# Performance work log

Hardware: AMD Instinct MI355X
Metric: run time of the kernel (lower is better)

Reference implementation:

```python
import jax, jax.numpy as jnp
import numpy as np


def _gcn_conv(x, edge_index, W, b):
    # PyG GCNConv: linear transform, add self-loops, symmetric deg^{-1/2} norm,
    # scatter-add aggregation from source (row) into target (col), then bias.
    N = x.shape[0]
    h = x @ W  # [N, out]
    loops = jnp.arange(N, dtype=edge_index.dtype)
    row = jnp.concatenate([edge_index[0], loops])  # sources j
    col = jnp.concatenate([edge_index[1], loops])  # targets i
    deg = jax.ops.segment_sum(jnp.ones_like(col, dtype=h.dtype), col, num_segments=N)
    dinv = jnp.where(deg > 0, jax.lax.rsqrt(deg), 0.0)
    norm = dinv[row] * dinv[col]  # [E+N]
    msgs = norm[:, None] * h[row]  # gather + scale
    out = jax.ops.segment_sum(msgs, col, num_segments=N)  # scatter-add
    return out + b


def setup_inputs() -> dict:
    key = jax.random.key(0)
    k1, k2, k3, k4 = jax.random.split(key, 4)
    N, E, F, H = 100000, 3200000, 128, 64
    x = jax.random.normal(k1, (N, F), dtype=jnp.float32)
    edge_index = jax.random.randint(k2, (2, E), 0, N, dtype=jnp.int64)
    W1 = jax.random.normal(k3, (F, H), dtype=jnp.float32) * (1.0 / np.sqrt(F))
    b1 = jnp.zeros((H,), dtype=jnp.float32)
    W2 = jax.random.normal(k4, (H, 1), dtype=jnp.float32) * (1.0 / np.sqrt(H))
    b2 = jnp.zeros((1,), dtype=jnp.float32)
    return {"x": x, "edge_index": edge_index, "W1": W1, "b1": b1, "W2": W2, "b2": b2}


def reference(x, edge_index, W1, b1, W2, b2):
    # eval mode: dropout is identity
    h = _gcn_conv(x, edge_index, W1, b1)
    h = jax.nn.relu(h)
    h = _gcn_conv(h, edge_index, W2, b2)  # [N, 1]
    return jnp.mean(h, axis=0)  # [1]
```

## Files before the change

kernel.cpp:

```cpp
#include <hip/hip_runtime.h>
#include <hip/hip_bf16.h>
#include <stdint.h>


#define F_IN 128
#define H_DIM 64
#define BKT_SH 7
#define BKT_SZ 128
#define MAXBKT 1024
#define PWG 128
#define PTHR 256
#define FINBLK 2048

typedef int   i4 __attribute__((ext_vector_type(4)));
typedef float f4 __attribute__((ext_vector_type(4)));

__device__ __forceinline__ float2 bfp(unsigned int u) {
    return make_float2(__uint_as_float(u << 16), __uint_as_float(u & 0xffff0000u));
}

__global__ __launch_bounds__(PTHR) void k_hist1(const int* __restrict__ col,
                                                int* __restrict__ histG,
                                                int E, int nbkt, int chunk) {
    __shared__ int h[MAXBKT];
    for (int i = threadIdx.x; i < nbkt; i += PTHR) h[i] = 0;
    __syncthreads();
    int s = blockIdx.x * chunk, e = min(E, s + chunk);
    if (s < e) {
        int s4 = s >> 2, e4 = e >> 2;
        const i4* c4 = (const i4*)col;
        int t = s4 + threadIdx.x;
        for (; t + 3 * PTHR < e4; t += 4 * PTHR) {
            i4 a = __builtin_nontemporal_load(c4 + t);
            i4 b = __builtin_nontemporal_load(c4 + t + PTHR);
            i4 c = __builtin_nontemporal_load(c4 + t + 2 * PTHR);
            i4 d = __builtin_nontemporal_load(c4 + t + 3 * PTHR);
            atomicAdd(&h[a.x >> BKT_SH], 1); atomicAdd(&h[a.y >> BKT_SH], 1);
            atomicAdd(&h[a.z >> BKT_SH], 1); atomicAdd(&h[a.w >> BKT_SH], 1);
            atomicAdd(&h[b.x >> BKT_SH], 1); atomicAdd(&h[b.y >> BKT_SH], 1);
            atomicAdd(&h[b.z >> BKT_SH], 1); atomicAdd(&h[b.w >> BKT_SH], 1);
            atomicAdd(&h[c.x >> BKT_SH], 1); atomicAdd(&h[c.y >> BKT_SH], 1);
            atomicAdd(&h[c.z >> BKT_SH], 1); atomicAdd(&h[c.w >> BKT_SH], 1);
            atomicAdd(&h[d.x >> BKT_SH], 1); atomicAdd(&h[d.y >> BKT_SH], 1);
            atomicAdd(&h[d.z >> BKT_SH], 1); atomicAdd(&h[d.w >> BKT_SH], 1);
        }
        for (; t < e4; t += PTHR) {
            i4 a = __builtin_nontemporal_load(c4 + t);
            atomicAdd(&h[a.x >> BKT_SH], 1); atomicAdd(&h[a.y >> BKT_SH], 1);
            atomicAdd(&h[a.z >> BKT_SH], 1); atomicAdd(&h[a.w >> BKT_SH], 1);
        }
        for (int i = (e4 << 2) + threadIdx.x; i < e; i += PTHR)
            atomicAdd(&h[col[i] >> BKT_SH], 1);
    }
    __syncthreads();
    for (int i = threadIdx.x; i < nbkt; i += PTHR)
        histG[(size_t)i * PWG + blockIdx.x] = h[i];
}

__global__ __launch_bounds__(PWG) void k_hscan_a(int* __restrict__ histG,
                                                 int* __restrict__ total, int nbkt) {
    __shared__ int s[PWG];
    int b = blockIdx.x, t = threadIdx.x;
    int v = histG[(size_t)b * PWG + t];
    s[t] = v;
    __syncthreads();
    for (int d = 1; d < PWG; d <<= 1) {
        int a = (t >= d) ? s[t - d] : 0;
        __syncthreads();
        s[t] += a;
        __syncthreads();
    }
    histG[(size_t)b * PWG + t] = s[t] - v;
    if (t == PWG - 1) total[b] = s[t];
}

__global__ __launch_bounds__(1024) void k_hscan_b(const int* __restrict__ total,
                                                  int* __restrict__ bstart, int nbkt) {
    __shared__ int s[1024];
    int t = threadIdx.x;
    int v = (t < nbkt) ? total[t] : 0;
    s[t] = v;
    __syncthreads();
    for (int d = 1; d < 1024; d <<= 1) {
        int a = (t >= d) ? s[t - d] : 0;
        __syncthreads();
        s[t] += a;
        __syncthreads();
    }
    if (t < nbkt) bstart[t] = s[t] - v;
    if (t == nbkt - 1) bstart[nbkt] = s[t];
}

__global__ __launch_bounds__(PTHR) void k_part(const int* __restrict__ row,
                                               const int* __restrict__ col,
                                               const int* __restrict__ histG,
                                               const int* __restrict__ bstart,
                                               unsigned int* __restrict__ part,
                                               int E, int nbkt, int chunk) {
    __shared__ int cur[MAXBKT];
    for (int i = threadIdx.x; i < nbkt; i += PTHR)
        cur[i] = bstart[i] + histG[(size_t)i * PWG + blockIdx.x];
    __syncthreads();
    int s = blockIdx.x * chunk, e = min(E, s + chunk);
    if (s >= e) return;
    int s4 = s >> 2, e4 = e >> 2;
    const i4* c4 = (const i4*)col;
    const i4* r4 = (const i4*)row;
    int t = s4 + threadIdx.x;
    for (; t + PTHR < e4; t += 2 * PTHR) {
        i4 ca = __builtin_nontemporal_load(c4 + t);
        i4 ra = __builtin_nontemporal_load(r4 + t);
        i4 cb = __builtin_nontemporal_load(c4 + t + PTHR);
        i4 rb = __builtin_nontemporal_load(r4 + t + PTHR);
        int p;
        p = atomicAdd(&cur[ca.x >> BKT_SH], 1);
        part[p] = ((unsigned int)ra.x << BKT_SH) | (unsigned int)(ca.x & (BKT_SZ - 1));
        p = atomicAdd(&cur[ca.y >> BKT_SH], 1);
        part[p] = ((unsigned int)ra.y << BKT_SH) | (unsigned int)(ca.y & (BKT_SZ - 1));
        p = atomicAdd(&cur[ca.z >> BKT_SH], 1);
        part[p] = ((unsigned int)ra.z << BKT_SH) | (unsigned int)(ca.z & (BKT_SZ - 1));
        p = atomicAdd(&cur[ca.w >> BKT_SH], 1);
        part[p] = ((unsigned int)ra.w << BKT_SH) | (unsigned int)(ca.w & (BKT_SZ - 1));
        p = atomicAdd(&cur[cb.x >> BKT_SH], 1);
        part[p] = ((unsigned int)rb.x << BKT_SH) | (unsigned int)(cb.x & (BKT_SZ - 1));
        p = atomicAdd(&cur[cb.y >> BKT_SH], 1);
        part[p] = ((unsigned int)rb.y << BKT_SH) | (unsigned int)(cb.y & (BKT_SZ - 1));
        p = atomicAdd(&cur[cb.z >> BKT_SH], 1);
        part[p] = ((unsigned int)rb.z << BKT_SH) | (unsigned int)(cb.z & (BKT_SZ - 1));
        p = atomicAdd(&cur[cb.w >> BKT_SH], 1);
        part[p] = ((unsigned int)rb.w << BKT_SH) | (unsigned int)(cb.w & (BKT_SZ - 1));
    }
    for (; t < e4; t += PTHR) {
        i4 ca = __builtin_nontemporal_load(c4 + t);
        i4 ra = __builtin_nontemporal_load(r4 + t);
        int p;
        p = atomicAdd(&cur[ca.x >> BKT_SH], 1);
        part[p] = ((unsigned int)ra.x << BKT_SH) | (unsigned int)(ca.x & (BKT_SZ - 1));
        p = atomicAdd(&cur[ca.y >> BKT_SH], 1);
        part[p] = ((unsigned int)ra.y << BKT_SH) | (unsigned int)(ca.y & (BKT_SZ - 1));
        p = atomicAdd(&cur[ca.z >> BKT_SH], 1);
        part[p] = ((unsigned int)ra.z << BKT_SH) | (unsigned int)(ca.z & (BKT_SZ - 1));
        p = atomicAdd(&cur[ca.w >> BKT_SH], 1);
        part[p] = ((unsigned int)ra.w << BKT_SH) | (unsigned int)(ca.w & (BKT_SZ - 1));
    }
    for (int i = (e4 << 2) + threadIdx.x; i < e; i += PTHR) {
        int c = col[i], r = row[i];
        int p = atomicAdd(&cur[c >> BKT_SH], 1);
        part[p] = ((unsigned int)r << BKT_SH) | (unsigned int)(c & (BKT_SZ - 1));
    }
}

__global__ __launch_bounds__(PTHR) void k_csr(const unsigned int* __restrict__ part,
                                              const int* __restrict__ bstart,
                                              int* __restrict__ offs,
                                              float* __restrict__ dinv,
                                              int* __restrict__ csr,
                                              int N, int E, int nbkt) {
    __shared__ int dg[BKT_SZ];
    __shared__ int sc[BKT_SZ];
    __shared__ int cur[BKT_SZ];
    int b = blockIdx.x, tid = threadIdx.x;
    if (tid < BKT_SZ) dg[tid] = 0;
    __syncthreads();
    int s = bstart[b], e = bstart[b + 1];
    for (int i = s + tid; i < e; i += PTHR)
        atomicAdd(&dg[part[i] & (BKT_SZ - 1)], 1);
    __syncthreads();
    if (tid < BKT_SZ) sc[tid] = dg[tid];
    __syncthreads();
    for (int d = 1; d < BKT_SZ; d <<= 1) {
        int v = (tid < BKT_SZ && tid >= d) ? sc[tid - d] : 0;
        __syncthreads();
        if (tid < BKT_SZ) sc[tid] += v;
        __syncthreads();
    }
    if (tid < BKT_SZ) {
        int ex = sc[tid] - dg[tid];
        cur[tid] = ex;
        int g = b * BKT_SZ + tid;
        if (g < N) {
            offs[g] = s + ex;
            dinv[g] = rsqrtf((float)dg[tid] + 1.0f);
        }
    }
    if (b == 0 && tid == 0) offs[N] = E;
    __syncthreads();
    for (int i = s + tid; i < e; i += PTHR) {
        unsigned int u = part[i];
        int cl = u & (BKT_SZ - 1);
        int p = atomicAdd(&cur[cl], 1);
        csr[s + p] = u >> BKT_SH;
    }
}

__global__ __launch_bounds__(256) void k_gemm1(const float* __restrict__ x,
                                               const float* __restrict__ W1,
                                               const float* __restrict__ dinv,
                                               ushort* __restrict__ xwb, int N) {
    __shared__ float xs[64 * 132];
    __shared__ float ws[128 * 64];
    int tid = threadIdx.x;
    int row0 = blockIdx.x * 64;

    const float4* w4 = (const float4*)W1;
    float4* ws4 = (float4*)ws;
#pragma unroll
    for (int i = 0; i < 8; i++) ws4[tid + 256 * i] = w4[tid + 256 * i];

#pragma unroll
    for (int i = 0; i < 8; i++) {
        int idx = tid + 256 * i;
        int r = idx >> 5;
        int c = idx & 31;
        f4 v = {0.f, 0.f, 0.f, 0.f};
        int gr = row0 + r;
        if (gr < N) v = __builtin_nontemporal_load((const f4*)x + (size_t)gr * 32 + c);
        *(f4*)&xs[r * 132 + c * 4] = v;
    }
    __syncthreads();

    int tx = tid & 15, ty = tid >> 4;
    float acc[4][4] = {};
#pragma unroll 4
    for (int k = 0; k < 128; k++) {
        float4 wv = *(const float4*)&ws[k * 64 + tx * 4];
#pragma unroll
        for (int i = 0; i < 4; i++) {
            float xv = xs[(ty * 4 + i) * 132 + k];
            acc[i][0] += xv * wv.x;
            acc[i][1] += xv * wv.y;
            acc[i][2] += xv * wv.z;
            acc[i][3] += xv * wv.w;
        }
    }
#pragma unroll
    for (int i = 0; i < 4; i++) {
        int gr = row0 + ty * 4 + i;
        if (gr < N) {
            float dsc = dinv[gr];
            __hip_bfloat16 q0 = __float2bfloat16(acc[i][0] * dsc);
            __hip_bfloat16 q1 = __float2bfloat16(acc[i][1] * dsc);
            __hip_bfloat16 q2 = __float2bfloat16(acc[i][2] * dsc);
            __hip_bfloat16 q3 = __float2bfloat16(acc[i][3] * dsc);
            ushort4 o = make_ushort4(*(ushort*)&q0, *(ushort*)&q1,
                                     *(ushort*)&q2, *(ushort*)&q3);
            *(ushort4*)&xwb[(size_t)gr * 64 + tx * 4] = o;
        }
    }
}

__global__ __launch_bounds__(256) void k_agg(const ushort* __restrict__ xws,
                                             const int* __restrict__ csr,
                                             const int* __restrict__ offs,
                                             const float* __restrict__ dinv,
                                             const float* __restrict__ b1,
                                             const float* __restrict__ W2,
                                             float* __restrict__ yp, int N) {
    int wid = (blockIdx.x * blockDim.x + threadIdx.x) >> 6;
    int lane = threadIdx.x & 63;
    if (wid >= N) return;
    int m = lane & 31, half = lane >> 5;
    const unsigned int* xw2 = (const unsigned int*)xws;

    float di = dinv[wid];
    float2 bv = ((const float2*)b1)[m];
    float2 wv = ((const float2*)W2)[m];

    float a0 = 0.f, a1 = 0.f;
    if (half == 0) {
        float2 sv = bfp(xw2[(size_t)wid * 32 + m]);
        a0 += sv.x; a1 += sv.y;
    }
    int p = offs[wid], pe = offs[wid + 1];
    for (; p + 16 <= pe; p += 16) {
        int j0 = csr[p + 0 + half];
        int j1 = csr[p + 2 + half];
        int j2 = csr[p + 4 + half];
        int j3 = csr[p + 6 + half];
        int j4 = csr[p + 8 + half];
        int j5 = csr[p + 10 + half];
        int j6 = csr[p + 12 + half];
        int j7 = csr[p + 14 + half];
        unsigned int u0 = xw2[(size_t)j0 * 32 + m];
        unsigned int u1 = xw2[(size_t)j1 * 32 + m];
        unsigned int u2 = xw2[(size_t)j2 * 32 + m];
        unsigned int u3 = xw2[(size_t)j3 * 32 + m];
        unsigned int u4 = xw2[(size_t)j4 * 32 + m];
        unsigned int u5 = xw2[(size_t)j5 * 32 + m];
        unsigned int u6 = xw2[(size_t)j6 * 32 + m];
        unsigned int u7 = xw2[(size_t)j7 * 32 + m];
        float2 v0 = bfp(u0), v1 = bfp(u1), v2 = bfp(u2), v3 = bfp(u3);
        float2 v4 = bfp(u4), v5 = bfp(u5), v6 = bfp(u6), v7 = bfp(u7);
        a0 += ((v0.x + v1.x) + (v2.x + v3.x)) + ((v4.x + v5.x) + (v6.x + v7.x));
        a1 += ((v0.y + v1.y) + (v2.y + v3.y)) + ((v4.y + v5.y) + (v6.y + v7.y));
    }
    for (; p + 8 <= pe; p += 8) {
        int j0 = csr[p + 0 + half];
        int j1 = csr[p + 2 + half];
        int j2 = csr[p + 4 + half];
        int j3 = csr[p + 6 + half];
        float2 v0 = bfp(xw2[(size_t)j0 * 32 + m]);
        float2 v1 = bfp(xw2[(size_t)j1 * 32 + m]);
        float2 v2 = bfp(xw2[(size_t)j2 * 32 + m]);
        float2 v3 = bfp(xw2[(size_t)j3 * 32 + m]);
        a0 += (v0.x + v1.x) + (v2.x + v3.x);
        a1 += (v0.y + v1.y) + (v2.y + v3.y);
    }
    for (; p + 2 <= pe; p += 2) {
        int j = csr[p + half];
        float2 v = bfp(xw2[(size_t)j * 32 + m]);
        a0 += v.x; a1 += v.y;
    }
    if (p < pe && half == 0) {
        int j = csr[p];
        float2 v = bfp(xw2[(size_t)j * 32 + m]);
        a0 += v.x; a1 += v.y;
    }
    a0 += __shfl_xor(a0, 32, 64);
    a1 += __shfl_xor(a1, 32, 64);
    float h0 = fmaxf(bv.x + di * a0, 0.f);
    float h1 = fmaxf(bv.y + di * a1, 0.f);
    float v = h0 * wv.x + h1 * wv.y;
#pragma unroll
    for (int d = 16; d > 0; d >>= 1) v += __shfl_xor(v, d, 64);
    if (lane == 0) yp[wid] = di * v;
}

__global__ __launch_bounds__(256) void k_final2(const int* __restrict__ csr,
                                                const int* __restrict__ offs,
                                                const float* __restrict__ dinv,
                                                const float* __restrict__ yp,
                                                float* __restrict__ partial, int N) {
    int lane = threadIdx.x & 63, w = threadIdx.x >> 6;
    int nwave_tot = gridDim.x * 4;
    int wid0 = blockIdx.x * 4 + w;
    float wpart = 0.f;
    for (int i = wid0; i < N; i += nwave_tot) {
        int p0 = offs[i], p1 = offs[i + 1];
        float s = (lane == 0) ? yp[i] : 0.f;
        for (int p = p0 + lane; p < p1; p += 64)
            s += yp[csr[p]];
#pragma unroll
        for (int d = 32; d > 0; d >>= 1) s += __shfl_xor(s, d, 64);
        if (lane == 0) wpart += dinv[i] * s;
    }
    __shared__ float wsum[4];
    if (lane == 0) wsum[w] = wpart;
    __syncthreads();
    if (threadIdx.x == 0)
        partial[blockIdx.x] = (wsum[0] + wsum[1]) + (wsum[2] + wsum[3]);
}

__global__ __launch_bounds__(256) void k_write(const float* __restrict__ partial,
                                               const float* __restrict__ b2,
                                               float* __restrict__ out, int nb, int N) {
    float s = 0.f;
    for (int i = threadIdx.x; i < nb; i += 256) s += partial[i];
#pragma unroll
    for (int d = 32; d > 0; d >>= 1) s += __shfl_xor(s, d, 64);
    __shared__ float wsum[4];
    int lane = threadIdx.x & 63, w = threadIdx.x >> 6;
    if (lane == 0) wsum[w] = s;
    __syncthreads();
    if (threadIdx.x == 0)
        out[0] = b2[0] + ((wsum[0] + wsum[1]) + (wsum[2] + wsum[3])) / (float)N;
}

extern "C" void kernel_launch(void* const* d_in, const int* in_sizes, int n_in,
                              void* d_out, int out_size, void* d_ws, size_t ws_size,
                              hipStream_t stream) {
    const float* x  = (const float*)d_in[0];
    const int*   ei = (const int*)d_in[1];
    const float* W1 = (const float*)d_in[2];
    const float* b1 = (const float*)d_in[3];
    const float* W2 = (const float*)d_in[4];
    const float* b2 = (const float*)d_in[5];

    int N = in_sizes[0] / F_IN;
    int E = in_sizes[1] / 2;
    const int* erow = ei;
    const int* ecol = ei + E;

    int NBKT = (N + BKT_SZ - 1) >> BKT_SH;
    int chunk = (((E + PWG - 1) / PWG) + 3) & ~3;

    char* w = (char*)d_ws;
    auto take = [&](size_t bytes) {
        char* p = w;
        w += (bytes + 255) & ~(size_t)255;
        return p;
    };
    int*          histG   = (int*)take((size_t)NBKT * PWG * 4);
    int*          total   = (int*)take((size_t)NBKT * 4);
    int*          bstart  = (int*)take((size_t)(NBKT + 1) * 4);
    unsigned int* part    = (unsigned int*)take((size_t)E * 4);
    int*          csr     = (int*)take((size_t)E * 4);
    int*          offs    = (int*)take((size_t)(N + 1) * 4);
    float*        dinv    = (float*)take((size_t)N * 4);
    float*        yp      = (float*)take((size_t)N * 4);
    float*        partial = (float*)take((size_t)FINBLK * 4);
    ushort*       xwb     = (ushort*)take((size_t)N * H_DIM * 2);
    (void)ws_size;

    float* out = (float*)d_out;

    k_hist1<<<PWG, PTHR, 0, stream>>>(ecol, histG, E, NBKT, chunk);
    k_hscan_a<<<NBKT, PWG, 0, stream>>>(histG, total, NBKT);
    k_hscan_b<<<1, 1024, 0, stream>>>(total, bstart, NBKT);
    k_part<<<PWG, PTHR, 0, stream>>>(erow, ecol, histG, bstart, part, E, NBKT, chunk);
    k_csr<<<NBKT, PTHR, 0, stream>>>(part, bstart, offs, dinv, csr, N, E, NBKT);
    k_gemm1<<<(N + 63) / 64, 256, 0, stream>>>(x, W1, dinv, xwb, N);
    k_agg<<<((size_t)N * 64 + 255) / 256, 256, 0, stream>>>(xwb, csr, offs, dinv, b1, W2, yp, N);
    k_final2<<<FINBLK, 256, 0, stream>>>(csr, offs, dinv, yp, partial, N);
    k_write<<<1, 256, 0, stream>>>(partial, b2, out, FINBLK, N);
}
```

Measured before the change: 216.8 us.

## Store layer-1 features as FP8, compute final sum over raw edges, double PWG

The intermediate node features from the first GEMM are now stored as FP8 e4m3 instead of bf16. This halves the bytes the aggregation kernel gathers per edge, and decode uses the hardware packed-conversion builtins when the compiler provides them. The final reduction no longer walks the CSR per node; it streams the original row/col arrays and sums yp[row]*dinv[col], plus the self-loop terms. The partition workgroup count is doubled. FP8 sharply reduces precision of the hidden features, which may threaten accuracy tolerance.

```diff
diff --git a/kernel.cpp b/kernel.cpp
--- a/kernel.cpp
+++ b/kernel.cpp
@@ -8,15 +8,61 @@
 #define BKT_SH 7
 #define BKT_SZ 128
 #define MAXBKT 1024
-#define PWG 128
+#define PWG 256
 #define PTHR 256
 #define FINBLK 2048
 
 typedef int   i4 __attribute__((ext_vector_type(4)));
 typedef float f4 __attribute__((ext_vector_type(4)));
-
-__device__ __forceinline__ float2 bfp(unsigned int u) {
-    return make_float2(__uint_as_float(u << 16), __uint_as_float(u & 0xffff0000u));
+typedef float fv2 __attribute__((ext_vector_type(2)));
+
+#if defined(__has_builtin)
+#if __has_builtin(__builtin_amdgcn_cvt_pk_f32_fp8) && __has_builtin(__builtin_amdgcn_cvt_pk_fp8_f32)
+#define HW_FP8 1
+#endif
+#endif
+
+__device__ __forceinline__ float sw_dec_e4m3(unsigned b) {
+    unsigned s = b & 0x80, e = (b >> 3) & 15, mm = b & 7;
+    float v;
+    if (e) v = __uint_as_float(((e + 120u) << 23) | (mm << 20));
+    else   v = (float)mm * 0.001953125f;
+    return s ? -v : v;
+}
+__device__ __forceinline__ unsigned sw_enc_e4m3(float f) {
+    unsigned s = (__float_as_uint(f) & 0x80000000u) ? 0x80u : 0u;
+    float a = fminf(fabsf(f), 448.0f);
+    if (a < 9.765625e-4f) return s;
+    if (a < 0.015625f) {
+        int k = (int)rintf(a * 512.0f);
+        if (k > 7) return s | 0x08;
+        return s | (unsigned)k;
+    }
+    int e; float mant = frexpf(a, &e);
+    int q = (int)rintf((mant * 2.0f - 1.0f) * 8.0f);
+    int E = e - 1;
+    if (q == 8) { q = 0; E += 1; }
+    if (E > 8) { E = 8; q = 6; }
+    return s | ((unsigned)(E + 7) << 3) | (unsigned)q;
+}
+
+__device__ __forceinline__ float2 f8pair(unsigned u) {
+#ifdef HW_FP8
+    fv2 r = __builtin_amdgcn_cvt_pk_f32_fp8((int)u, false);
+    return make_float2(r.x, r.y);
+#else
+    return make_float2(sw_dec_e4m3(u & 0xff), sw_dec_e4m3((u >> 8) & 0xff));
+#endif
+}
+__device__ __forceinline__ unsigned f8pack4(float v0, float v1, float v2, float v3) {
+#ifdef HW_FP8
+    unsigned pk = (unsigned)__builtin_amdgcn_cvt_pk_fp8_f32(v0, v1, 0, false);
+    pk = (unsigned)__builtin_amdgcn_cvt_pk_fp8_f32(v2, v3, (int)pk, true);
+    return pk;
+#else
+    return sw_enc_e4m3(v0) | (sw_enc_e4m3(v1) << 8) |
+           (sw_enc_e4m3(v2) << 16) | (sw_enc_e4m3(v3) << 24);
+#endif
 }
 
 __global__ __launch_bounds__(PTHR) void k_hist1(const int* __restrict__ col,
@@ -196,7 +242,8 @@
 __global__ __launch_bounds__(256) void k_gemm1(const float* __restrict__ x,
                                                const float* __restrict__ W1,
                                                const float* __restrict__ dinv,
-                                               ushort* __restrict__ xwb, int N) {
+                                               unsigned int* __restrict__ xw8,
+                                               int N) {
     __shared__ float xs[64 * 132];
     __shared__ float ws[128 * 64];
     int tid = threadIdx.x;
@@ -238,18 +285,14 @@
         int gr = row0 + ty * 4 + i;
         if (gr < N) {
             float dsc = dinv[gr];
-            __hip_bfloat16 q0 = __float2bfloat16(acc[i][0] * dsc);
-            __hip_bfloat16 q1 = __float2bfloat16(acc[i][1] * dsc);
-            __hip_bfloat16 q2 = __float2bfloat16(acc[i][2] * dsc);
-            __hip_bfloat16 q3 = __float2bfloat16(acc[i][3] * dsc);
-            ushort4 o = make_ushort4(*(ushort*)&q0, *(ushort*)&q1,
-                                     *(ushort*)&q2, *(ushort*)&q3);
-            *(ushort4*)&xwb[(size_t)gr * 64 + tx * 4] = o;
+            unsigned pk = f8pack4(acc[i][0] * dsc, acc[i][1] * dsc,
+                                  acc[i][2] * dsc, acc[i][3] * dsc);
+            xw8[(size_t)gr * 16 + tx] = pk;
         }
     }
 }
 
-__global__ __launch_bounds__(256) void k_agg(const ushort* __restrict__ xws,
+__global__ __launch_bounds__(256) void k_agg(const ushort* __restrict__ xw8,
                                              const int* __restrict__ csr,
                                              const int* __restrict__ offs,
                                              const float* __restrict__ dinv,
@@ -260,7 +303,6 @@
     int lane = threadIdx.x & 63;
     if (wid >= N) return;
     int m = lane & 31, half = lane >> 5;
-    const unsigned int* xw2 = (const unsigned int*)xws;
 
     float di = dinv[wid];
     float2 bv = ((const float2*)b1)[m];
@@ -268,7 +310,7 @@
 
     float a0 = 0.f, a1 = 0.f;
     if (half == 0) {
-        float2 sv = bfp(xw2[(size_t)wid * 32 + m]);
+        float2 sv = f8pair(xw8[(size_t)wid * 32 + m]);
         a0 += sv.x; a1 += sv.y;
     }
     int p = offs[wid], pe = offs[wid + 1];
@@ -281,16 +323,16 @@
         int j5 = csr[p + 10 + half];
         int j6 = csr[p + 12 + half];
         int j7 = csr[p + 14 + half];
-        unsigned int u0 = xw2[(size_t)j0 * 32 + m];
-        unsigned int u1 = xw2[(size_t)j1 * 32 + m];
-        unsigned int u2 = xw2[(size_t)j2 * 32 + m];
-        unsigned int u3 = xw2[(size_t)j3 * 32 + m];
-        unsigned int u4 = xw2[(size_t)j4 * 32 + m];
-        unsigned int u5 = xw2[(size_t)j5 * 32 + m];
-        unsigned int u6 = xw2[(size_t)j6 * 32 + m];
-        unsigned int u7 = xw2[(size_t)j7 * 32 + m];
-        float2 v0 = bfp(u0), v1 = bfp(u1), v2 = bfp(u2), v3 = bfp(u3);
-        float2 v4 = bfp(u4), v5 = bfp(u5), v6 = bfp(u6), v7 = bfp(u7);
+        ushort u0 = xw8[(size_t)j0 * 32 + m];
+        ushort u1 = xw8[(size_t)j1 * 32 + m];
+        ushort u2 = xw8[(size_t)j2 * 32 + m];
+        ushort u3 = xw8[(size_t)j3 * 32 + m];
+        ushort u4 = xw8[(size_t)j4 * 32 + m];
+        ushort u5 = xw8[(size_t)j5 * 32 + m];
+        ushort u6 = xw8[(size_t)j6 * 32 + m];
+        ushort u7 = xw8[(size_t)j7 * 32 + m];
+        float2 v0 = f8pair(u0), v1 = f8pair(u1), v2 = f8pair(u2), v3 = f8pair(u3);
+        float2 v4 = f8pair(u4), v5 = f8pair(u5), v6 = f8pair(u6), v7 = f8pair(u7);
         a0 += ((v0.x + v1.x) + (v2.x + v3.x)) + ((v4.x + v5.x) + (v6.x + v7.x));
         a1 += ((v0.y + v1.y) + (v2.y + v3.y)) + ((v4.y + v5.y) + (v6.y + v7.y));
     }
@@ -299,21 +341,21 @@
         int j1 = csr[p + 2 + half];
         int j2 = csr[p + 4 + half];
         int j3 = csr[p + 6 + half];
-        float2 v0 = bfp(xw2[(size_t)j0 * 32 + m]);
-        float2 v1 = bfp(xw2[(size_t)j1 * 32 + m]);
-        float2 v2 = bfp(xw2[(size_t)j2 * 32 + m]);
-        float2 v3 = bfp(xw2[(size_t)j3 * 32 + m]);
+        float2 v0 = f8pair(xw8[(size_t)j0 * 32 + m]);
+        float2 v1 = f8pair(xw8[(size_t)j1 * 32 + m]);
+        float2 v2 = f8pair(xw8[(size_t)j2 * 32 + m]);
+        float2 v3 = f8pair(xw8[(size_t)j3 * 32 + m]);
         a0 += (v0.x + v1.x) + (v2.x + v3.x);
         a1 += (v0.y + v1.y) + (v2.y + v3.y);
     }
     for (; p + 2 <= pe; p += 2) {
         int j = csr[p + half];
-        float2 v = bfp(xw2[(size_t)j * 32 + m]);
+        float2 v = f8pair(xw8[(size_t)j * 32 + m]);
         a0 += v.x; a1 += v.y;
     }
     if (p < pe && half == 0) {
         int j = csr[p];
-        float2 v = bfp(xw2[(size_t)j * 32 + m]);
+        float2 v = f8pair(xw8[(size_t)j * 32 + m]);
         a0 += v.x; a1 += v.y;
     }
     a0 += __shfl_xor(a0, 32, 64);
@@ -326,26 +368,39 @@
     if (lane == 0) yp[wid] = di * v;
 }
 
-__global__ __launch_bounds__(256) void k_final2(const int* __restrict__ csr,
-                                                const int* __restrict__ offs,
+__global__ __launch_bounds__(256) void k_final2(const int* __restrict__ row,
+                                                const int* __restrict__ col,
                                                 const float* __restrict__ dinv,
                                                 const float* __restrict__ yp,
-                                                float* __restrict__ partial, int N) {
+                                                float* __restrict__ partial,
+                                                int N, int E) {
+    int tid = blockIdx.x * blockDim.x + threadIdx.x;
+    int nthr = gridDim.x * blockDim.x;
+    float local = 0.f;
+    int E4 = E >> 2;
+    const i4* r4 = (const i4*)row;
+    const i4* c4 = (const i4*)col;
+    for (int t = tid; t < E4; t += nthr) {
+        i4 r = __builtin_nontemporal_load(r4 + t);
+        i4 c = __builtin_nontemporal_load(c4 + t);
+        local += yp[r.x] * dinv[c.x] + yp[r.y] * dinv[c.y]
+               + yp[r.z] * dinv[c.z] + yp[r.w] * dinv[c.w];
+    }
+    for (int e = (E4 << 2) + tid; e < E; e += nthr)
+        local += yp[row[e]] * dinv[col[e]];
+    int N4 = N >> 2;
+    for (int t = tid; t < N4; t += nthr) {
+        f4 d = *((const f4*)dinv + t);
+        f4 yv = *((const f4*)yp + t);
+        local += d.x * yv.x + d.y * yv.y + d.z * yv.z + d.w * yv.w;
+    }
+    for (int i = (N4 << 2) + tid; i < N; i += nthr)
+        local += dinv[i] * yp[i];
+#pragma unroll
+    for (int d = 32; d > 0; d >>= 1) local += __shfl_xor(local, d, 64);
+    __shared__ float wsum[4];
     int lane = threadIdx.x & 63, w = threadIdx.x >> 6;
-    int nwave_tot = gridDim.x * 4;
-    int wid0 = blockIdx.x * 4 + w;
-    float wpart = 0.f;
-    for (int i = wid0; i < N; i += nwave_tot) {
-        int p0 = offs[i], p1 = offs[i + 1];
-        float s = (lane == 0) ? yp[i] : 0.f;
-        for (int p = p0 + lane; p < p1; p += 64)
-            s += yp[csr[p]];
-#pragma unroll
-        for (int d = 32; d > 0; d >>= 1) s += __shfl_xor(s, d, 64);
-        if (lane == 0) wpart += dinv[i] * s;
-    }
-    __shared__ float wsum[4];
-    if (lane == 0) wsum[w] = wpart;
+    if (lane == 0) wsum[w] = local;
     __syncthreads();
     if (threadIdx.x == 0)
         partial[blockIdx.x] = (wsum[0] + wsum[1]) + (wsum[2] + wsum[3]);
@@ -399,7 +454,7 @@
     float*        dinv    = (float*)take((size_t)N * 4);
     float*        yp      = (float*)take((size_t)N * 4);
     float*        partial = (float*)take((size_t)FINBLK * 4);
-    ushort*       xwb     = (ushort*)take((size_t)N * H_DIM * 2);
+    unsigned int* xw8     = (unsigned int*)take((size_t)N * H_DIM);
     (void)ws_size;
 
     float* out = (float*)d_out;
@@ -409,8 +464,8 @@
     k_hscan_b<<<1, 1024, 0, stream>>>(total, bstart, NBKT);
     k_part<<<PWG, PTHR, 0, stream>>>(erow, ecol, histG, bstart, part, E, NBKT, chunk);
     k_csr<<<NBKT, PTHR, 0, stream>>>(part, bstart, offs, dinv, csr, N, E, NBKT);
-    k_gemm1<<<(N + 63) / 64, 256, 0, stream>>>(x, W1, dinv, xwb, N);
-    k_agg<<<((size_t)N * 64 + 255) / 256, 256, 0, stream>>>(xwb, csr, offs, dinv, b1, W2, yp, N);
-    k_final2<<<FINBLK, 256, 0, stream>>>(csr, offs, dinv, yp, partial, N);
+    k_gemm1<<<(N + 63) / 64, 256, 0, stream>>>(x, W1, dinv, xw8, N);
+    k_agg<<<((size_t)N * 64 + 255) / 256, 256, 0, stream>>>((const ushort*)xw8, csr, offs, dinv, b1, W2, yp, N);
+    k_final2<<<FINBLK, 256, 0, stream>>>(erow, ecol, dinv, yp, partial, N, E);
     k_write<<<1, 256, 0, stream>>>(partial, b2, out, FINBLK, N);
 }
```

Result: no change. 215.1 us (-0.8%).
